# Optimization experiments

Hardware: AMD Instinct MI355X
Metric: run time of the kernel (lower is better)

## Reference

```python
import jax, jax.numpy as jnp
import numpy as np

N, E = 10000, 320000
F_N, F_E, F_G, LATENT, F_OUT = 128, 128, 32, 128, 128


def _make_mlp_params(key, dims):
    # dims: list of layer widths, e.g. [256,128,128,128,256]
    params = []
    for i in range(len(dims) - 1):
        key, k1, k2 = jax.random.split(key, 3)
        lim = 1.0 / np.sqrt(dims[i])
        w = jax.random.uniform(k1, (dims[i], dims[i + 1]), jnp.float32, -lim, lim)
        b = jax.random.uniform(k2, (dims[i + 1],), jnp.float32, -lim, lim)
        params.append((w, b))
    return params, key


def _mlp(h, ws, bs, activate_final):
    n = len(ws)
    for i in range(n):
        h = h @ ws[i] + bs[i]
        if i < n - 1 or activate_final:
            h = jax.nn.relu(h)
    return h


def setup_inputs() -> dict:
    key = jax.random.key(0)
    key, kx, ke, kg, ki = jax.random.split(key, 5)
    x = jax.random.normal(kx, (N, F_N), jnp.float32)
    edge_index = jax.random.randint(ki, (2, E), 0, N, jnp.int64)
    edge_attr = jax.random.normal(ke, (E, F_E), jnp.float32)
    global_attr = jax.random.normal(kg, (1, F_G), jnp.float32)

    # node_mlp_1: (F_N+F_E) -> L -> L -> L -> (F_N+F_E), activate_final=True
    p1, key = _make_mlp_params(key, [F_N + F_E, LATENT, LATENT, LATENT, F_N + F_E])
    # node_mlp_2: (2*F_N+F_E+F_G) -> L -> L -> L -> F_OUT, activate_final=False
    p2, key = _make_mlp_params(key, [2 * F_N + F_E + F_G, LATENT, LATENT, LATENT, F_OUT])

    inp = {"x": x, "edge_index": edge_index, "edge_attr": edge_attr, "global_attr": global_attr}
    for i, (w, b) in enumerate(p1):
        inp[f"m1_w{i}"] = w
        inp[f"m1_b{i}"] = b
    for i, (w, b) in enumerate(p2):
        inp[f"m2_w{i}"] = w
        inp[f"m2_b{i}"] = b
    return inp


def reference(x, edge_index, edge_attr, global_attr,
              m1_w0, m1_b0, m1_w1, m1_b1, m1_w2, m1_b2, m1_w3, m1_b3,
              m2_w0, m2_b0, m2_w1, m2_b1, m2_w2, m2_b2, m2_w3, m2_b3):
    row, col = edge_index[0], edge_index[1]
    n = x.shape[0]
    # gather sender-side node feats, per-edge MLP (activate_final=True)
    h = jnp.concatenate([x[row], edge_attr], axis=1)          # [E, F_N+F_E]
    h = _mlp(h, [m1_w0, m1_w1, m1_w2, m1_w3], [m1_b0, m1_b1, m1_b2, m1_b3], True)
    # scatter_mean over destination nodes
    s = jax.ops.segment_sum(h, col, num_segments=n)           # [N, F_N+F_E]
    cnt = jax.ops.segment_sum(jnp.ones((h.shape[0],), h.dtype), col, num_segments=n)
    agg = s / jnp.maximum(cnt, 1.0)[:, None]
    # repeat global feats to N rows (pad_to_size mode='repeat', G divides N)
    g = jnp.tile(global_attr, (n // global_attr.shape[0], 1))  # [N, F_G]
    out = jnp.concatenate([x, agg, g], axis=1)                 # [N, 2F_N+F_E+F_G]
    return _mlp(out, [m2_w0, m2_w1, m2_w2, m2_w3], [m2_b0, m2_b1, m2_b2, m2_b3], False)
```

## Files before the change

### kernel.cpp

```cpp
#include <hip/hip_runtime.h>
#include <hip/hip_bf16.h>

#define E_EDGES 320000
#define N_NODES 10000

typedef __attribute__((ext_vector_type(8))) short short8;
typedef __attribute__((ext_vector_type(4))) float floatx4;

__device__ __forceinline__ float bf2f(unsigned short u) {
    union { unsigned int i; float f; } v; v.i = ((unsigned int)u) << 16; return v.f;
}
__device__ __forceinline__ unsigned int pk2(float a, float b) {
    float2 t; t.x = a; t.y = b;
    __hip_bfloat162 h = __float22bfloat162_rn(t);
    union { __hip_bfloat162 h; unsigned int u; } c; c.h = h; return c.u;
}

template<int KT, int FT>
__device__ __forceinline__ void load_a(const unsigned short* __restrict__ wt, int ntiles, int t0,
                                       int lane, short8 (&a)[KT][FT])
{
#pragma unroll
    for (int kt = 0; kt < KT; ++kt)
#pragma unroll
        for (int ft = 0; ft < FT; ++ft)
            a[kt][ft] = *(const short8*)&wt[(size_t)(kt * ntiles + t0 + ft) * 512 + lane * 8];
}

template<int K, int FT, int ET>
__device__ __forceinline__ void layer_mfma(const unsigned short* __restrict__ in, int istride,
                                           int lane, const short8 (&a)[K / 32][FT],
                                           floatx4 (&acc)[FT][ET])
{
    constexpr int KT = K / 32;
    const int quad = lane >> 4;
    const int mrow = lane & 15;
    floatx4 zero = {0.f, 0.f, 0.f, 0.f};
#pragma unroll
    for (int ft = 0; ft < FT; ++ft)
#pragma unroll
        for (int et = 0; et < ET; ++et)
            acc[ft][et] = zero;

#pragma unroll
    for (int kt = 0; kt < KT; ++kt) {
        const int koff = kt * 32 + quad * 8;
        short8 b[ET];
#pragma unroll
        for (int et = 0; et < ET; ++et)
            b[et] = *(const short8*)&in[(et * 16 + mrow) * istride + koff];
#pragma unroll
        for (int ft = 0; ft < FT; ++ft)
#pragma unroll
            for (int et = 0; et < ET; ++et)
                acc[ft][et] = __builtin_amdgcn_mfma_f32_16x16x32_bf16(a[kt][ft], b[et], acc[ft][et], 0, 0, 0);
    }
}

template<int K, int Nn, int ET>
__device__ __forceinline__ void layer_stream(const unsigned short* __restrict__ in, int istride,
                                             const unsigned short* __restrict__ wt,
                                             int lane, int n0, floatx4 (&acc)[2][ET])
{
    constexpr int KT = K / 32;
    const int quad = lane >> 4;
    const int mrow = lane & 15;

    floatx4 zero = {0.f, 0.f, 0.f, 0.f};
#pragma unroll
    for (int ft = 0; ft < 2; ++ft)
#pragma unroll
        for (int et = 0; et < ET; ++et)
            acc[ft][et] = zero;

    short8 a[2][2];
    short8 b[2][ET];
#pragma unroll
    for (int ft = 0; ft < 2; ++ft)
        a[0][ft] = *(const short8*)&wt[(size_t)((n0 >> 4) + ft) * 512 + lane * 8];
#pragma unroll
    for (int et = 0; et < ET; ++et)
        b[0][et] = *(const short8*)&in[(et * 16 + mrow) * istride + quad * 8];

#pragma unroll
    for (int kt = 0; kt < KT; ++kt) {
        if (kt + 1 < KT) {
            const int nb = (kt + 1) & 1;
            const int koff = (kt + 1) * 32 + quad * 8;
#pragma unroll
            for (int ft = 0; ft < 2; ++ft)
                a[nb][ft] = *(const short8*)&wt[(size_t)((kt + 1) * (Nn >> 4) + (n0 >> 4) + ft) * 512 + lane * 8];
#pragma unroll
            for (int et = 0; et < ET; ++et)
                b[nb][et] = *(const short8*)&in[(et * 16 + mrow) * istride + koff];
        }
#pragma unroll
        for (int ft = 0; ft < 2; ++ft)
#pragma unroll
            for (int et = 0; et < ET; ++et)
                acc[ft][et] = __builtin_amdgcn_mfma_f32_16x16x32_bf16(a[kt & 1][ft], b[kt & 1][et], acc[ft][et], 0, 0, 0);
    }
}

template<int FT, int ET>
__device__ __forceinline__ void store_lds(floatx4 (&acc)[FT][ET], const float* __restrict__ bias,
                                          int lane, int n0, unsigned short* __restrict__ out, int ostride,
                                          bool relu)
{
    const int quad = lane >> 4, mrow = lane & 15;
#pragma unroll
    for (int ft = 0; ft < FT; ++ft) {
        int fbase = n0 + ft * 16 + quad * 4;
        float4 bv = *(const float4*)&bias[fbase];
#pragma unroll
        for (int et = 0; et < ET; ++et) {
            int edge = et * 16 + mrow;
            float v0 = acc[ft][et][0] + bv.x;
            float v1 = acc[ft][et][1] + bv.y;
            float v2 = acc[ft][et][2] + bv.z;
            float v3 = acc[ft][et][3] + bv.w;
            if (relu) {
                v0 = v0 > 0.f ? v0 : 0.f; v1 = v1 > 0.f ? v1 : 0.f;
                v2 = v2 > 0.f ? v2 : 0.f; v3 = v3 > 0.f ? v3 : 0.f;
            }
            uint2 pk; pk.x = pk2(v0, v1); pk.y = pk2(v2, v3);
            *(uint2*)&out[edge * ostride + fbase] = pk;
        }
    }
}

struct TDesc { const float* src; unsigned short* dst; int nElem; int logN; int blockStart; };
struct TArgs { TDesc d[8]; };

__global__ void prep_kernel(TArgs a, const int* __restrict__ eidx, int* __restrict__ cnt, int histStart)
{
    int b = blockIdx.x;
    if (b >= histStart) {
        int e = (b - histStart) * 256 + threadIdx.x;
        if (e < E_EDGES) atomicAdd(&cnt[eidx[E_EDGES + e]], 1);
        return;
    }
    int i = 0;
#pragma unroll
    for (int j = 1; j < 8; ++j)
        if (b >= a.d[j].blockStart) i = j;
    const TDesc t = a.d[i];
    int idx = (b - t.blockStart) * 256 + threadIdx.x;
    if (idx < t.nElem) {
        int n = idx & ((1 << t.logN) - 1);
        int k = idx >> t.logN;
        int ntiles = 1 << (t.logN - 4);
        size_t dsti = ((size_t)(k >> 5) * ntiles + (n >> 4)) * 512
                    + ((k >> 3) & 3) * 128 + (n & 15) * 8 + (k & 7);
        union { float f; unsigned int u; } c; c.f = t.src[idx];
        unsigned int uu = c.u;
        t.dst[dsti] = (unsigned short)((uu + 0x7fffu + ((uu >> 16) & 1u)) >> 16);
    }
}

__global__ void scan_kernel(const int* __restrict__ cnt, int* __restrict__ fill)
{
    __shared__ int partial[256];
    const int CH = 40;
    int tid = threadIdx.x;
    int base = tid * CH;
    int local[CH];
    int sum = 0;
#pragma unroll
    for (int j = 0; j < CH; ++j) {
        int idx = base + j;
        int c = (idx < N_NODES) ? cnt[idx] : 0;
        local[j] = c;
        sum += c;
    }
    partial[tid] = sum;
    __syncthreads();
    for (int o = 1; o < 256; o <<= 1) {
        int v = (tid >= o) ? partial[tid - o] : 0;
        __syncthreads();
        partial[tid] += v;
        __syncthreads();
    }
    int run = partial[tid] - sum;
#pragma unroll
    for (int j = 0; j < CH; ++j) {
        int idx = base + j;
        if (idx < N_NODES) fill[idx] = run;
        run += local[j];
    }
}

__global__ void fill_kernel(const int* __restrict__ eidx, int* __restrict__ fill,
                            int4* __restrict__ pack)
{
    int e = blockIdx.x * 256 + threadIdx.x;
    int c = eidx[E_EDGES + e];
    int r = eidx[e];
    int pos = atomicAdd(&fill[c], 1);
    pack[pos] = make_int4(e, r, c, 0);
}

__global__ __launch_bounds__(256, 4) void edge_kernel(
    const float* __restrict__ x,
    const float* __restrict__ ea,
    const int4* __restrict__ pack,
    const unsigned short* __restrict__ wt0, const float* __restrict__ b0,
    const unsigned short* __restrict__ wt1, const float* __restrict__ b1,
    const unsigned short* __restrict__ wt2, const float* __restrict__ b2,
    const unsigned short* __restrict__ wt3, const float* __restrict__ b3,
    float* __restrict__ s)
{
    __shared__ __align__(16) char U[25600];
    __shared__ int es[32];
    __shared__ int rs[32];
    __shared__ int ds[32];

    unsigned short* H0 = (unsigned short*)U;
    unsigned short* H1 = (unsigned short*)(U + 16896);
    unsigned short* H2 = (unsigned short*)U;
    unsigned short* H3 = H1;
    unsigned short* G  = (unsigned short*)U;

    const int tid = threadIdx.x;
    const int p0 = blockIdx.x * 32;

    if (tid < 32) {
        int4 pr = pack[p0 + tid];
        es[tid] = pr.x; rs[tid] = pr.y; ds[tid] = pr.z;
    }
    __syncthreads();

    const int lane = tid & 63;
    const int wave = tid >> 6;
    const int t32 = wave * 2;

    float4 v[8];
#pragma unroll
    for (int i = 0; i < 8; ++i) {
        int task = tid + i * 256;
        int row = task >> 6, part = task & 63;
        const float* src = (part < 32) ? (x  + (size_t)rs[row] * 128 + part * 4)
                                       : (ea + (size_t)es[row] * 128 + (part - 32) * 4);
        v[i] = *(const float4*)src;
    }
    __builtin_amdgcn_sched_barrier(0);
    short8 a0[8][2];
    load_a<8, 2>(wt0, 8, t32, lane, a0);
    __builtin_amdgcn_sched_barrier(0);
#pragma unroll
    for (int i = 0; i < 8; ++i) {
        int task = tid + i * 256;
        int row = task >> 6, part = task & 63;
        uint2 pk; pk.x = pk2(v[i].x, v[i].y); pk.y = pk2(v[i].z, v[i].w);
        *(uint2*)&H0[row * 264 + part * 4] = pk;
    }
    __syncthreads();

    short8 a1[4][2];
    load_a<4, 2>(wt1, 8, t32, lane, a1);
    __builtin_amdgcn_sched_barrier(0);
    {
        floatx4 acc[2][2];
        layer_mfma<256, 2, 2>(H0, 264, lane, a0, acc);
        store_lds<2, 2>(acc, b0, lane, wave * 32, H1, 136, true);
    }
    __syncthreads();

    short8 a2[4][2];
    load_a<4, 2>(wt2, 8, t32, lane, a2);
    __builtin_amdgcn_sched_barrier(0);
    {
        floatx4 acc[2][2];
        layer_mfma<128, 2, 2>(H1, 136, lane, a1, acc);
        store_lds<2, 2>(acc, b1, lane, wave * 32, H2, 136, true);
    }
    __syncthreads();

    short8 a3[4][4];
    load_a<4, 4>(wt3, 16, wave * 4, lane, a3);
    __builtin_amdgcn_sched_barrier(0);
    {
        floatx4 acc[2][2];
        layer_mfma<128, 2, 2>(H2, 136, lane, a2, acc);
        store_lds<2, 2>(acc, b2, lane, wave * 32, H3, 136, true);
    }
    __syncthreads();

    {
        floatx4 acc[4][2];
        layer_mfma<128, 4, 2>(H3, 136, lane, a3, acc);
        store_lds<4, 2>(acc, b3, lane, wave * 64, G, 264, true);
    }
    __syncthreads();

    {
        int p = tid & 127;
        int half = tid >> 7;
        int col2 = p * 2;
        int base = half * 16;
        float s0 = 0.f, s1 = 0.f;
#pragma unroll 4
        for (int i = 0; i < 16; ++i) {
            int gi = base + i;
            unsigned int u = *(const unsigned int*)&G[gi * 264 + col2];
            s0 += bf2f((unsigned short)u);
            s1 += bf2f((unsigned short)(u >> 16));
            if (i == 15 || ds[gi + 1] != ds[gi]) {
                float* dst = &s[(size_t)ds[gi] * 256 + col2];
                atomicAdd(dst, s0);
                atomicAdd(dst + 1, s1);
                s0 = 0.f; s1 = 0.f;
            }
        }
    }
}

__global__ __launch_bounds__(256, 2) void node_kernel(
    const float* __restrict__ x,
    const float* __restrict__ g,
    const float* __restrict__ s,
    const int* __restrict__ cnt,
    const unsigned short* __restrict__ wt0, const float* __restrict__ b0,
    const unsigned short* __restrict__ wt1, const float* __restrict__ b1,
    const unsigned short* __restrict__ wt2, const float* __restrict__ b2,
    const unsigned short* __restrict__ wt3, const float* __restrict__ b3,
    float* __restrict__ out)
{
    __shared__ __align__(16) char NU[17920];
    unsigned short* Abig = (unsigned short*)NU;
    unsigned short* HsA  = (unsigned short*)(NU + 13568);
    unsigned short* HsB  = (unsigned short*)NU;

    const int tid = threadIdx.x;
    const int node0 = blockIdx.x * 16;

#pragma unroll
    for (int i = 0; i < 2; ++i) {
        int task = tid + i * 256;
        int row = task >> 5, part = task & 31;
        float4 v = *(const float4*)(x + (size_t)(node0 + row) * 128 + part * 4);
        uint2 pk; pk.x = pk2(v.x, v.y); pk.y = pk2(v.z, v.w);
        *(uint2*)&Abig[row * 424 + part * 4] = pk;
    }
#pragma unroll
    for (int i = 0; i < 4; ++i) {
        int task = tid + i * 256;
        int row = task >> 6, part = task & 63;
        int node = node0 + row;
        float c = (float)cnt[node];
        float inv = 1.f / (c > 1.f ? c : 1.f);
        floatx4 v = *(const floatx4*)(s + (size_t)node * 256 + part * 4);
        uint2 pk;
        pk.x = pk2(v[0] * inv, v[1] * inv);
        pk.y = pk2(v[2] * inv, v[3] * inv);
        *(uint2*)&Abig[row * 424 + 128 + part * 4] = pk;
    }
    if (tid < 128) {
        int row = tid >> 3, part = tid & 7;
        float4 v = *(const float4*)(g + part * 4);
        uint2 pk; pk.x = pk2(v.x, v.y); pk.y = pk2(v.z, v.w);
        *(uint2*)&Abig[row * 424 + 384 + part * 4] = pk;
    }
    __syncthreads();

    const int lane = tid & 63;
    const int wave = tid >> 6;
    const int t32 = wave * 2;

    short8 a1[4][2];
    load_a<4, 2>(wt1, 8, t32, lane, a1);
    __builtin_amdgcn_sched_barrier(0);
    {
        floatx4 acc[2][1];
        layer_stream<416, 128, 1>(Abig, 424, wt0, lane, wave * 32, acc);
        store_lds<2, 1>(acc, b0, lane, wave * 32, HsA, 136, true);
    }
    __syncthreads();

    short8 a2[4][2];
    load_a<4, 2>(wt2, 8, t32, lane, a2);
    __builtin_amdgcn_sched_barrier(0);
    {
        floatx4 acc[2][1];
        layer_mfma<128, 2, 1>(HsA, 136, lane, a1, acc);
        store_lds<2, 1>(acc, b1, lane, wave * 32, HsB, 136, true);
    }
    __syncthreads();

    short8 a3[4][2];
    load_a<4, 2>(wt3, 8, t32, lane, a3);
    __builtin_amdgcn_sched_barrier(0);
    {
        floatx4 acc[2][1];
        layer_mfma<128, 2, 1>(HsB, 136, lane, a2, acc);
        store_lds<2, 1>(acc, b2, lane, wave * 32, HsA, 136, true);
    }
    __syncthreads();

    {
        floatx4 acc[2][1];
        layer_mfma<128, 2, 1>(HsA, 136, lane, a3, acc);
        const int quad = lane >> 4, mrow = lane & 15;
#pragma unroll
        for (int ft = 0; ft < 2; ++ft) {
            int fbase = wave * 32 + ft * 16 + quad * 4;
            float4 bv = *(const float4*)&b3[fbase];
            int node = node0 + mrow;
            float4 o;
            o.x = acc[ft][0][0] + bv.x;
            o.y = acc[ft][0][1] + bv.y;
            o.z = acc[ft][0][2] + bv.z;
            o.w = acc[ft][0][3] + bv.w;
            *(float4*)&out[(size_t)node * 128 + fbase] = o;
        }
    }
}

extern "C" void kernel_launch(void* const* d_in, const int* in_sizes, int n_in,
                              void* d_out, int out_size, void* d_ws, size_t ws_size,
                              hipStream_t stream)
{
    (void)in_sizes; (void)n_in; (void)out_size; (void)ws_size;

    const float* x  = (const float*)d_in[0];
    const int* eidx = (const int*)d_in[1];
    const float* ea = (const float*)d_in[2];
    const float* g  = (const float*)d_in[3];

    const float* w1[4]  = { (const float*)d_in[4],  (const float*)d_in[6],
                            (const float*)d_in[8],  (const float*)d_in[10] };
    const float* bb1[4] = { (const float*)d_in[5],  (const float*)d_in[7],
                            (const float*)d_in[9],  (const float*)d_in[11] };
    const float* w2[4]  = { (const float*)d_in[12], (const float*)d_in[14],
                            (const float*)d_in[16], (const float*)d_in[18] };
    const float* bb2[4] = { (const float*)d_in[13], (const float*)d_in[15],
                            (const float*)d_in[17], (const float*)d_in[19] };

    char* p = (char*)d_ws;
    unsigned short* wt1_0 = (unsigned short*)p; p += 256 * 128 * 2;
    unsigned short* wt1_1 = (unsigned short*)p; p += 128 * 128 * 2;
    unsigned short* wt1_2 = (unsigned short*)p; p += 128 * 128 * 2;
    unsigned short* wt1_3 = (unsigned short*)p; p += 128 * 256 * 2;
    unsigned short* wt2_0 = (unsigned short*)p; p += 416 * 128 * 2;
    unsigned short* wt2_1 = (unsigned short*)p; p += 128 * 128 * 2;
    unsigned short* wt2_2 = (unsigned short*)p; p += 128 * 128 * 2;
    unsigned short* wt2_3 = (unsigned short*)p; p += 128 * 128 * 2;
    float* s    = (float*)p; p += (size_t)N_NODES * 256 * 4;
    int* cnt    = (int*)p;   p += (size_t)N_NODES * 4;
    int* fill   = (int*)p;   p += (size_t)N_NODES * 4;
    int4* pack  = (int4*)p;  p += (size_t)E_EDGES * 16;

    hipMemsetAsync(s, 0, (size_t)N_NODES * 256 * 4 + (size_t)N_NODES * 4, stream);

    TArgs ta;
    int bs = 0;
    auto set = [&](int i, const float* src, unsigned short* dst, int K, int Nn, int logN) {
        ta.d[i].src = src; ta.d[i].dst = dst; ta.d[i].nElem = K * Nn;
        ta.d[i].logN = logN; ta.d[i].blockStart = bs;
        bs += (K * Nn + 255) / 256;
    };
    set(0, w1[0], wt1_0, 256, 128, 7);
    set(1, w1[1], wt1_1, 128, 128, 7);
    set(2, w1[2], wt1_2, 128, 128, 7);
    set(3, w1[3], wt1_3, 128, 256, 8);
    set(4, w2[0], wt2_0, 416, 128, 7);
    set(5, w2[1], wt2_1, 128, 128, 7);
    set(6, w2[2], wt2_2, 128, 128, 7);
    set(7, w2[3], wt2_3, 128, 128, 7);

    int histBlocks = E_EDGES / 256;
    hipLaunchKernelGGL(prep_kernel, dim3(bs + histBlocks), dim3(256), 0, stream,
                       ta, eidx, cnt, bs);
    hipLaunchKernelGGL(scan_kernel, dim3(1), dim3(256), 0, stream, cnt, fill);
    hipLaunchKernelGGL(fill_kernel, dim3(E_EDGES / 256), dim3(256), 0, stream,
                       eidx, fill, pack);

    hipLaunchKernelGGL(edge_kernel, dim3(E_EDGES / 32), dim3(256), 0, stream,
                       x, ea, pack,
                       wt1_0, bb1[0], wt1_1, bb1[1], wt1_2, bb1[2], wt1_3, bb1[3],
                       s);

    hipLaunchKernelGGL(node_kernel, dim3(N_NODES / 16), dim3(256), 0, stream,
                       x, g, s, cnt,
                       wt2_0, bb2[0], wt2_1, bb2[1], wt2_2, bb2[2], wt2_3, bb2[3],
                       (float*)d_out);
}
```

Measured before the change: 424.4 us.

## Process 64 edges per block with split-K layer0 and halved output layer

The edge kernel now handles 64 edges per block instead of 32. The first layer's K=256 is split into x and edge_attr halves that share one 128-wide LDS buffer, and the final 256-wide layer runs as two 128-column passes, each followed by its own segmented atomic scatter. Together these keep LDS at two 136-stride buffers while raising the MFMA edge tile to 4, so each weight fragment is reused over more edges. Zeroing of the sum buffer moves out of a memset into extra blocks of the prep kernel. The costs are more accumulator registers, more barriers, and a second scatter pass per block.

New measurement: 510.4 us. 20.3% more time.

```diff
diff --git a/kernel.cpp b/kernel.cpp
--- a/kernel.cpp
+++ b/kernel.cpp
@@ -18,16 +18,16 @@
 
 template<int KT, int FT>
 __device__ __forceinline__ void load_a(const unsigned short* __restrict__ wt, int ntiles, int t0,
-                                       int lane, short8 (&a)[KT][FT])
+                                       int kt0, int lane, short8 (&a)[KT][FT])
 {
 #pragma unroll
     for (int kt = 0; kt < KT; ++kt)
 #pragma unroll
         for (int ft = 0; ft < FT; ++ft)
-            a[kt][ft] = *(const short8*)&wt[(size_t)(kt * ntiles + t0 + ft) * 512 + lane * 8];
-}
-
-template<int K, int FT, int ET>
+            a[kt][ft] = *(const short8*)&wt[(size_t)((kt0 + kt) * ntiles + t0 + ft) * 512 + lane * 8];
+}
+
+template<int K, int FT, int ET, bool ZERO>
 __device__ __forceinline__ void layer_mfma(const unsigned short* __restrict__ in, int istride,
                                            int lane, const short8 (&a)[K / 32][FT],
                                            floatx4 (&acc)[FT][ET])
@@ -35,13 +35,14 @@
     constexpr int KT = K / 32;
     const int quad = lane >> 4;
     const int mrow = lane & 15;
-    floatx4 zero = {0.f, 0.f, 0.f, 0.f};
-#pragma unroll
-    for (int ft = 0; ft < FT; ++ft)
-#pragma unroll
-        for (int et = 0; et < ET; ++et)
-            acc[ft][et] = zero;
-
+    if (ZERO) {
+        floatx4 zero = {0.f, 0.f, 0.f, 0.f};
+#pragma unroll
+        for (int ft = 0; ft < FT; ++ft)
+#pragma unroll
+            for (int et = 0; et < ET; ++et)
+                acc[ft][et] = zero;
+    }
 #pragma unroll
     for (int kt = 0; kt < KT; ++kt) {
         const int koff = kt * 32 + quad * 8;
@@ -132,9 +133,16 @@
 struct TDesc { const float* src; unsigned short* dst; int nElem; int logN; int blockStart; };
 struct TArgs { TDesc d[8]; };
 
-__global__ void prep_kernel(TArgs a, const int* __restrict__ eidx, int* __restrict__ cnt, int histStart)
+__global__ void prep_kernel(TArgs a, const int* __restrict__ eidx, int* __restrict__ cnt,
+                            float4* __restrict__ s4, int histStart, int zeroStart)
 {
     int b = blockIdx.x;
+    if (b >= zeroStart) {
+        int idx = (b - zeroStart) * 256 + threadIdx.x;
+        float4 z = {0.f, 0.f, 0.f, 0.f};
+        s4[idx] = z;
+        return;
+    }
     if (b >= histStart) {
         int e = (b - histStart) * 256 + threadIdx.x;
         if (e < E_EDGES) atomicAdd(&cnt[eidx[E_EDGES + e]], 1);
@@ -210,21 +218,18 @@
     const unsigned short* __restrict__ wt3, const float* __restrict__ b3,
     float* __restrict__ s)
 {
-    __shared__ __align__(16) char U[25600];
-    __shared__ int es[32];
-    __shared__ int rs[32];
-    __shared__ int ds[32];
-
-    unsigned short* H0 = (unsigned short*)U;
-    unsigned short* H1 = (unsigned short*)(U + 16896);
-    unsigned short* H2 = (unsigned short*)U;
-    unsigned short* H3 = H1;
-    unsigned short* G  = (unsigned short*)U;
+    __shared__ __align__(16) char U[34816];
+    __shared__ int es[64];
+    __shared__ int rs[64];
+    __shared__ int ds[64];
+
+    unsigned short* A = (unsigned short*)U;
+    unsigned short* B = (unsigned short*)(U + 17408);
 
     const int tid = threadIdx.x;
-    const int p0 = blockIdx.x * 32;
-
-    if (tid < 32) {
+    const int p0 = blockIdx.x * 64;
+
+    if (tid < 64) {
         int4 pr = pack[p0 + tid];
         es[tid] = pr.x; rs[tid] = pr.y; ds[tid] = pr.z;
     }
@@ -233,80 +238,131 @@
     const int lane = tid & 63;
     const int wave = tid >> 6;
     const int t32 = wave * 2;
-
-    float4 v[8];
+    const int quad = lane >> 4, mrow = lane & 15;
+
+    float4 vx[8], ve[8];
 #pragma unroll
     for (int i = 0; i < 8; ++i) {
         int task = tid + i * 256;
-        int row = task >> 6, part = task & 63;
-        const float* src = (part < 32) ? (x  + (size_t)rs[row] * 128 + part * 4)
-                                       : (ea + (size_t)es[row] * 128 + (part - 32) * 4);
-        v[i] = *(const float4*)src;
-    }
-    __builtin_amdgcn_sched_barrier(0);
-    short8 a0[8][2];
-    load_a<8, 2>(wt0, 8, t32, lane, a0);
-    __builtin_amdgcn_sched_barrier(0);
+        int row = task >> 5, part = task & 31;
+        vx[i] = *(const float4*)(x + (size_t)rs[row] * 128 + part * 4);
+    }
 #pragma unroll
     for (int i = 0; i < 8; ++i) {
         int task = tid + i * 256;
-        int row = task >> 6, part = task & 63;
-        uint2 pk; pk.x = pk2(v[i].x, v[i].y); pk.y = pk2(v[i].z, v[i].w);
-        *(uint2*)&H0[row * 264 + part * 4] = pk;
+        int row = task >> 5, part = task & 31;
+        ve[i] = *(const float4*)(ea + (size_t)es[row] * 128 + part * 4);
+    }
+    __builtin_amdgcn_sched_barrier(0);
+    short8 a0a[4][2];
+    load_a<4, 2>(wt0, 8, t32, 0, lane, a0a);
+    __builtin_amdgcn_sched_barrier(0);
+#pragma unroll
+    for (int i = 0; i < 8; ++i) {
+        int task = tid + i * 256;
+        int row = task >> 5, part = task & 31;
+        uint2 pk; pk.x = pk2(vx[i].x, vx[i].y); pk.y = pk2(vx[i].z, vx[i].w);
+        *(uint2*)&A[row * 136 + part * 4] = pk;
+    }
+    __syncthreads();
+
+    floatx4 acc[2][4];
+    layer_mfma<128, 2, 4, true>(A, 136, lane, a0a, acc);
+    __builtin_amdgcn_sched_barrier(0);
+    short8 a0b[4][2];
+    load_a<4, 2>(wt0, 8, t32, 4, lane, a0b);
+    __builtin_amdgcn_sched_barrier(0);
+    __syncthreads();
+
+#pragma unroll
+    for (int i = 0; i < 8; ++i) {
+        int task = tid + i * 256;
+        int row = task >> 5, part = task & 31;
+        uint2 pk; pk.x = pk2(ve[i].x, ve[i].y); pk.y = pk2(ve[i].z, ve[i].w);
+        *(uint2*)&A[row * 136 + part * 4] = pk;
     }
     __syncthreads();
 
     short8 a1[4][2];
-    load_a<4, 2>(wt1, 8, t32, lane, a1);
-    __builtin_amdgcn_sched_barrier(0);
-    {
-        floatx4 acc[2][2];
-        layer_mfma<256, 2, 2>(H0, 264, lane, a0, acc);
-        store_lds<2, 2>(acc, b0, lane, wave * 32, H1, 136, true);
-    }
+    load_a<4, 2>(wt1, 8, t32, 0, lane, a1);
+    __builtin_amdgcn_sched_barrier(0);
+    layer_mfma<128, 2, 4, false>(A, 136, lane, a0b, acc);
+    store_lds<2, 4>(acc, b0, lane, wave * 32, B, 136, true);
     __syncthreads();
 
     short8 a2[4][2];
-    load_a<4, 2>(wt2, 8, t32, lane, a2);
-    __builtin_amdgcn_sched_barrier(0);
-    {
-        floatx4 acc[2][2];
-        layer_mfma<128, 2, 2>(H1, 136, lane, a1, acc);
-        store_lds<2, 2>(acc, b1, lane, wave * 32, H2, 136, true);
-    }
-    __syncthreads();
-
-    short8 a3[4][4];
-    load_a<4, 4>(wt3, 16, wave * 4, lane, a3);
-    __builtin_amdgcn_sched_barrier(0);
-    {
-        floatx4 acc[2][2];
-        layer_mfma<128, 2, 2>(H2, 136, lane, a2, acc);
-        store_lds<2, 2>(acc, b2, lane, wave * 32, H3, 136, true);
-    }
-    __syncthreads();
-
-    {
-        floatx4 acc[4][2];
-        layer_mfma<128, 4, 2>(H3, 136, lane, a3, acc);
-        store_lds<4, 2>(acc, b3, lane, wave * 64, G, 264, true);
-    }
-    __syncthreads();
-
-    {
-        int p = tid & 127;
-        int half = tid >> 7;
-        int col2 = p * 2;
-        int base = half * 16;
+    load_a<4, 2>(wt2, 8, t32, 0, lane, a2);
+    __builtin_amdgcn_sched_barrier(0);
+    {
+        floatx4 acc1[2][4];
+        layer_mfma<128, 2, 4, true>(B, 136, lane, a1, acc1);
+        store_lds<2, 4>(acc1, b1, lane, wave * 32, A, 136, true);
+    }
+    __syncthreads();
+
+    short8 a3a[4][2];
+    load_a<4, 2>(wt3, 16, t32, 0, lane, a3a);
+    __builtin_amdgcn_sched_barrier(0);
+    {
+        floatx4 acc2[2][4];
+        layer_mfma<128, 2, 4, true>(A, 136, lane, a2, acc2);
+        store_lds<2, 4>(acc2, b2, lane, wave * 32, B, 136, true);
+    }
+    __syncthreads();
+
+    {
+        floatx4 acc3[2][4];
+        layer_mfma<128, 2, 4, true>(B, 136, lane, a3a, acc3);
+        store_lds<2, 4>(acc3, b3, lane, wave * 32, A, 136, true);
+    }
+    __syncthreads();
+
+    short8 a3b[4][2];
+    load_a<4, 2>(wt3, 16, 8 + t32, 0, lane, a3b);
+    __builtin_amdgcn_sched_barrier(0);
+    {
+        int colp = tid & 63;
+        int seg  = tid >> 6;
+        int col2 = colp * 2;
+        int base = seg * 16;
         float s0 = 0.f, s1 = 0.f;
 #pragma unroll 4
         for (int i = 0; i < 16; ++i) {
             int gi = base + i;
-            unsigned int u = *(const unsigned int*)&G[gi * 264 + col2];
+            unsigned int u = *(const unsigned int*)&A[gi * 136 + col2];
             s0 += bf2f((unsigned short)u);
             s1 += bf2f((unsigned short)(u >> 16));
             if (i == 15 || ds[gi + 1] != ds[gi]) {
                 float* dst = &s[(size_t)ds[gi] * 256 + col2];
+                atomicAdd(dst, s0);
+                atomicAdd(dst + 1, s1);
+                s0 = 0.f; s1 = 0.f;
+            }
+        }
+    }
+    __syncthreads();
+
+    {
+        floatx4 acc3[2][4];
+        layer_mfma<128, 2, 4, true>(B, 136, lane, a3b, acc3);
+        store_lds<2, 4>(acc3, b3 + 128, lane, wave * 32, A, 136, true);
+    }
+    __syncthreads();
+
+    {
+        int colp = tid & 63;
+        int seg  = tid >> 6;
+        int col2 = colp * 2;
+        int base = seg * 16;
+        float s0 = 0.f, s1 = 0.f;
+#pragma unroll 4
+        for (int i = 0; i < 16; ++i) {
+            int gi = base + i;
+            unsigned int u = *(const unsigned int*)&A[gi * 136 + col2];
+            s0 += bf2f((unsigned short)u);
+            s1 += bf2f((unsigned short)(u >> 16));
+            if (i == 15 || ds[gi + 1] != ds[gi]) {
+                float* dst = &s[(size_t)ds[gi] * 256 + 128 + col2];
                 atomicAdd(dst, s0);
                 atomicAdd(dst + 1, s1);
                 s0 = 0.f; s1 = 0.f;
@@ -368,7 +424,7 @@
     const int t32 = wave * 2;
 
     short8 a1[4][2];
-    load_a<4, 2>(wt1, 8, t32, lane, a1);
+    load_a<4, 2>(wt1, 8, t32, 0, lane, a1);
     __builtin_amdgcn_sched_barrier(0);
     {
         floatx4 acc[2][1];
@@ -378,28 +434,28 @@
     __syncthreads();
 
     short8 a2[4][2];
-    load_a<4, 2>(wt2, 8, t32, lane, a2);
+    load_a<4, 2>(wt2, 8, t32, 0, lane, a2);
     __builtin_amdgcn_sched_barrier(0);
     {
         floatx4 acc[2][1];
-        layer_mfma<128, 2, 1>(HsA, 136, lane, a1, acc);
+        layer_mfma<128, 2, 1, true>(HsA, 136, lane, a1, acc);
         store_lds<2, 1>(acc, b1, lane, wave * 32, HsB, 136, true);
     }
     __syncthreads();
 
     short8 a3[4][2];
-    load_a<4, 2>(wt3, 8, t32, lane, a3);
+    load_a<4, 2>(wt3, 8, t32, 0, lane, a3);
     __builtin_amdgcn_sched_barrier(0);
     {
         floatx4 acc[2][1];
-        layer_mfma<128, 2, 1>(HsB, 136, lane, a2, acc);
+        layer_mfma<128, 2, 1, true>(HsB, 136, lane, a2, acc);
         store_lds<2, 1>(acc, b2, lane, wave * 32, HsA, 136, true);
     }
     __syncthreads();
 
     {
         floatx4 acc[2][1];
-        layer_mfma<128, 2, 1>(HsA, 136, lane, a3, acc);
+        layer_mfma<128, 2, 1, true>(HsA, 136, lane, a3, acc);
         const int quad = lane >> 4, mrow = lane & 15;
 #pragma unroll
         for (int ft = 0; ft < 2; ++ft) {
@@ -450,7 +506,7 @@
     int* fill   = (int*)p;   p += (size_t)N_NODES * 4;
     int4* pack  = (int4*)p;  p += (size_t)E_EDGES * 16;
 
-    hipMemsetAsync(s, 0, (size_t)N_NODES * 256 * 4 + (size_t)N_NODES * 4, stream);
+    hipMemsetAsync(cnt, 0, (size_t)N_NODES * 4, stream);
 
     TArgs ta;
     int bs = 0;
@@ -469,13 +525,14 @@
     set(7, w2[3], wt2_3, 128, 128, 7);
 
     int histBlocks = E_EDGES / 256;
-    hipLaunchKernelGGL(prep_kernel, dim3(bs + histBlocks), dim3(256), 0, stream,
-                       ta, eidx, cnt, bs);
+    int zeroBlocks = (N_NODES * 256 / 4) / 256;
+    hipLaunchKernelGGL(prep_kernel, dim3(bs + histBlocks + zeroBlocks), dim3(256), 0, stream,
+                       ta, eidx, cnt, (float4*)s, bs, bs + histBlocks);
     hipLaunchKernelGGL(scan_kernel, dim3(1), dim3(256), 0, stream, cnt, fill);
     hipLaunchKernelGGL(fill_kernel, dim3(E_EDGES / 256), dim3(256), 0, stream,
                        eidx, fill, pack);
 
-    hipLaunchKernelGGL(edge_kernel, dim3(E_EDGES / 32), dim3(256), 0, stream,
+    hipLaunchKernelGGL(edge_kernel, dim3(E_EDGES / 64), dim3(256), 0, stream,
                        x, ea, pack,
                        wt1_0, bb1[0], wt1_1, bb1[1], wt1_2, bb1[2], wt1_3, bb1[3],
                        s);
```
